# Kernel optimization log

Measured on AMD Instinct MI355X. Metric: run time of the kernel, lower is better.

## Reference

```python
import jax, jax.numpy as jnp
import numpy as np

B, T, D, K = 8, 4096, 1024, 4096

def setup_inputs() -> dict:
    key = jax.random.key(0)
    kx, kc = jax.random.split(key)
    x = jax.random.normal(kx, (B, T, D), dtype=jnp.float32)
    C = jax.random.normal(kc, (D, K), dtype=jnp.float32)  # centroids stored as [d, K]
    Cnorm = jnp.sum(C * C, axis=0, keepdims=True)  # [1, K], matches torch precompute
    return {"x": x, "C": C, "Cnorm": Cnorm}

def reference(x, C, Cnorm):
    batched = x.ndim == 3
    if batched:
        b, t, d = x.shape
        x2 = x.reshape(-1, d)  # [N, d]
    else:
        x2 = x
    dist = jnp.sum(x2 * x2, axis=1, keepdims=True) - 2.0 * (x2 @ C) + Cnorm
    assigned = jnp.argmin(dist, axis=1)
    if batched:
        assigned = assigned.reshape(b, t)
    return assigned
```

## Files before the change

### kernel.cpp

```cpp
#include <hip/hip_runtime.h>
#include <cstdint>
#include <cstddef>

typedef _Float16 half8 __attribute__((ext_vector_type(8)));
typedef _Float16 half4 __attribute__((ext_vector_type(4)));
typedef float    floatx4 __attribute__((ext_vector_type(4)));

constexpr int N_ROWS = 32768;
constexpr int D_DIM  = 1024;
constexpr int K_CENT = 4096;
constexpr int CAP    = 4096;
constexpr int KSL    = 4;
constexpr int RSL    = 8;
constexpr float EPS_GAP = 0.4f;

__device__ __forceinline__ void gload_lds16(const void* g, void* l) {
    __builtin_amdgcn_global_load_lds(
        (const __attribute__((address_space(1))) uint32_t*)g,
        (__attribute__((address_space(3))) uint32_t*)l, 16, 0, 0);
}

__global__ __launch_bounds__(256) void convert_C_kernel(
    const float* __restrict__ C, _Float16* __restrict__ ChiT, _Float16* __restrict__ CloT)
{
    __shared__ float tile[32][33];
    const int bk = blockIdx.x, bd = blockIdx.y, t = threadIdx.x;
    const int r = t >> 3, c4 = (t & 7) * 4;
    const float4 v = *(const float4*)&C[(size_t)(bd * 32 + r) * K_CENT + bk * 32 + c4];
    tile[r][c4 + 0] = v.x; tile[r][c4 + 1] = v.y;
    tile[r][c4 + 2] = v.z; tile[r][c4 + 3] = v.w;
    __syncthreads();
    half4 h, l;
#pragma unroll
    for (int i = 0; i < 4; ++i) {
        const float f = tile[c4 + i][r];
        const _Float16 hi = (_Float16)f;
        h[i] = hi;
        l[i] = (_Float16)(f - (float)hi);
    }
    *(half4*)&ChiT[(size_t)(bk * 32 + r) * D_DIM + bd * 32 + c4] = h;
    *(half4*)&CloT[(size_t)(bk * 32 + r) * D_DIM + bd * 32 + c4] = l;
}

__global__ __launch_bounds__(256) void convert_x_kernel(
    const float* __restrict__ x, _Float16* __restrict__ xh)
{
    const size_t g = (size_t)blockIdx.x * 256 + threadIdx.x;
    const float4 v0 = *(const float4*)&x[g * 8];
    const float4 v1 = *(const float4*)&x[g * 8 + 4];
    half8 h;
    h[0] = (_Float16)v0.x; h[1] = (_Float16)v0.y; h[2] = (_Float16)v0.z; h[3] = (_Float16)v0.w;
    h[4] = (_Float16)v1.x; h[5] = (_Float16)v1.y; h[6] = (_Float16)v1.z; h[7] = (_Float16)v1.w;
    *(half8*)&xh[g * 8] = h;
}

constexpr int Q_A  = 0;
constexpr int Q_B  = 4096;
constexpr int Q_HB = 8192;

__device__ __forceinline__ void stage4(
    _Float16* buf, const _Float16* __restrict__ xh, const _Float16* __restrict__ ChiT,
    int row0, int kc, int kd, int wid, int scol, int skg)
{
#pragma unroll
    for (int q = 0; q < 2; ++q) {
        const int sub = wid * 2 + q;
        gload_lds16(&xh[(size_t)(row0 + sub * 16 + scol) * D_DIM + kd + skg * 8],
                    buf + Q_A + sub * 512);
    }
#pragma unroll
    for (int q = 0; q < 2; ++q) {
        const int sub = wid * 2 + q;
        gload_lds16(&ChiT[(size_t)(kc + sub * 16 + scol) * D_DIM + kd + skg * 8],
                    buf + Q_B + sub * 512);
    }
}

__global__ __launch_bounds__(256, 3) void kmeans_pass1(
    const _Float16* __restrict__ xh, const _Float16* __restrict__ ChiT,
    const float* __restrict__ Cnorm,
    float* __restrict__ m1buf, int* __restrict__ i1buf, float* __restrict__ m2buf)
{
    __shared__ _Float16 lds[2][Q_HB];
    __shared__ float red_d[2][64][2];
    __shared__ int   red_i[2][64][2];
    __shared__ float red_2[2][64][2];

    const int bid  = blockIdx.x;
    const int xcd  = bid & 7;
    const int ks   = xcd & 3;
    const int rb   = (bid >> 3) * 2 + (xcd >> 2);
    const int row0 = rb * 128;
    const int kb0  = ks * (K_CENT / KSL);

    const int tid  = threadIdx.x;
    const int lane = tid & 63;
    const int wid  = tid >> 6;
    const int wm   = wid >> 1;
    const int wn   = wid & 1;

    const int l15 = lane & 15;
    const int l4  = lane >> 4;
    const int kge = l4 ^ ((l15 >> 1) & 3);
    const int fragoff = l15 * 32 + kge * 8;

    const int scol = lane >> 2;
    const int skg  = (lane & 3) ^ ((scol >> 1) & 3);

    float rm1 = 3.4e38f, rm2 = 3.4e38f;
    int   ri1 = 0;

    constexpr int NCH   = (K_CENT / KSL) / 128;
    constexpr int NSTEP = NCH * 32;

    stage4(lds[0], xh, ChiT, row0, kb0, 0, wid, scol, skg);

    floatx4 acc[4][4];
#pragma unroll
    for (int i = 0; i < 4; ++i)
#pragma unroll
        for (int j = 0; j < 4; ++j) acc[i][j] = (floatx4)0.0f;

    for (int s = 0; s < NSTEP; ++s) {
        _Float16* bufc = lds[s & 1];
        _Float16* bufn = lds[(s + 1) & 1];
        const int s1 = s + 1;
        if (s1 < NSTEP) {
            const int nkc = kb0 + (s1 >> 5) * 128;
            const int nkd = (s1 & 31) * 32;
            stage4(bufn, xh, ChiT, row0, nkc, nkd, wid, scol, skg);
            asm volatile("s_waitcnt vmcnt(4)" ::: "memory");
        } else {
            asm volatile("s_waitcnt vmcnt(0)" ::: "memory");
        }
        __builtin_amdgcn_s_barrier();

        half8 ah[4], bh[4];
#pragma unroll
        for (int i = 0; i < 4; ++i)
            ah[i] = *(const half8*)(bufc + Q_A + (wm * 4 + i) * 512 + fragoff);
#pragma unroll
        for (int j = 0; j < 4; ++j)
            bh[j] = *(const half8*)(bufc + Q_B + (wn * 4 + j) * 512 + fragoff);

        __builtin_amdgcn_s_setprio(1);
#pragma unroll
        for (int i = 0; i < 4; ++i)
#pragma unroll
            for (int j = 0; j < 4; ++j)
                acc[i][j] = __builtin_amdgcn_mfma_f32_16x16x32_f16(ah[i], bh[j], acc[i][j], 0, 0, 0);
        __builtin_amdgcn_s_setprio(0);

        asm volatile("" ::: "memory");
        __builtin_amdgcn_s_barrier();

        if ((s & 31) == 31) {
            const int ci   = s >> 5;
            const int colw = ci * 128 + wn * 64;
            float cn4[4];
#pragma unroll
            for (int j = 0; j < 4; ++j) cn4[j] = Cnorm[kb0 + colw + j * 16 + l15];

#pragma unroll
            for (int i = 0; i < 4; ++i)
#pragma unroll
                for (int r = 0; r < 4; ++r) {
                    float m1 = 3.4e38f, m2 = 3.4e38f;
                    int   i1 = 0;
#pragma unroll
                    for (int j = 0; j < 4; ++j) {
                        const float d  = fmaf(-2.0f, acc[i][j][r], cn4[j]);
                        const int   ix = kb0 + colw + j * 16 + l15;
                        if (d < m1) { m2 = m1; m1 = d; i1 = ix; }
                        else if (d < m2) { m2 = d; }
                    }
#pragma unroll
                    for (int off = 1; off < 16; off <<= 1) {
                        const float om1 = __shfl_xor(m1, off, 64);
                        const int   oi  = __shfl_xor(i1, off, 64);
                        const float om2 = __shfl_xor(m2, off, 64);
                        const float nm2 = fminf(fminf(m2, om2), fmaxf(m1, om1));
                        if (om1 < m1 || (om1 == m1 && oi < i1)) { m1 = om1; i1 = oi; }
                        m2 = nm2;
                    }
                    if (l15 == 0) {
                        const int rr = i * 16 + l4 * 4 + r;
                        red_d[wm][rr][wn] = m1;
                        red_i[wm][rr][wn] = i1;
                        red_2[wm][rr][wn] = m2;
                    }
                }
            asm volatile("s_waitcnt lgkmcnt(0)" ::: "memory");
            __builtin_amdgcn_s_barrier();
            __builtin_amdgcn_sched_barrier(0);

            if (tid < 128) {
                const int h2 = tid >> 6;
                const int r2 = tid & 63;
                float m1 = red_d[h2][r2][0], m2 = red_2[h2][r2][0];
                int   i1 = red_i[h2][r2][0];
                const float om1 = red_d[h2][r2][1];
                const int   oi  = red_i[h2][r2][1];
                const float om2 = red_2[h2][r2][1];
                m2 = fminf(fminf(m2, om2), fmaxf(m1, om1));
                if (om1 < m1 || (om1 == m1 && oi < i1)) { m1 = om1; i1 = oi; }
                const float nm2 = fminf(fminf(rm2, m2), fmaxf(rm1, m1));
                if (m1 < rm1 || (m1 == rm1 && i1 < ri1)) { rm1 = m1; ri1 = i1; }
                rm2 = nm2;
            }

#pragma unroll
            for (int i = 0; i < 4; ++i)
#pragma unroll
                for (int j = 0; j < 4; ++j) acc[i][j] = (floatx4)0.0f;
        }
    }

    if (tid < 128) {
        const size_t off = (size_t)ks * N_ROWS + row0 + tid;
        m1buf[off] = rm1;
        i1buf[off] = ri1;
        m2buf[off] = rm2;
    }
}

__global__ __launch_bounds__(256) void kmeans_merge4(
    const float* __restrict__ m1buf, const int* __restrict__ i1buf,
    const float* __restrict__ m2buf, int* __restrict__ out,
    int* __restrict__ urows, unsigned int* __restrict__ ucount)
{
    const int row = blockIdx.x * 256 + threadIdx.x;
    float m1 = m1buf[row], m2 = m2buf[row];
    int   i1 = i1buf[row];
#pragma unroll
    for (int s = 1; s < KSL; ++s) {
        const float om1 = m1buf[(size_t)s * N_ROWS + row];
        const float om2 = m2buf[(size_t)s * N_ROWS + row];
        const int   oi  = i1buf[(size_t)s * N_ROWS + row];
        const float nm2 = fminf(fminf(m2, om2), fmaxf(m1, om1));
        if (om1 < m1 || (om1 == m1 && oi < i1)) { m1 = om1; i1 = oi; }
        m2 = nm2;
    }
    out[row] = i1;
    if (m2 - m1 <= EPS_GAP) {
        const unsigned slot = atomicAdd(ucount, 1u);
        if (slot < (unsigned)CAP) urows[slot] = row;
    }
}

__global__ __launch_bounds__(64) void kmeans_gather(
    const float* __restrict__ x, const int* __restrict__ urows,
    const unsigned int* __restrict__ ucount,
    _Float16* __restrict__ xch, _Float16* __restrict__ xcl)
{
    const unsigned cntr = *ucount;
    const unsigned cnt = cntr > (unsigned)CAP ? (unsigned)CAP : cntr;
    const unsigned slot = blockIdx.x;
    if (slot >= cnt) return;
    const int row = urows[slot];
    const int t = threadIdx.x;
#pragma unroll
    for (int e = 0; e < 16; ++e) {
        const int idx = e * 64 + t;
        const float v = x[(size_t)row * D_DIM + idx];
        const _Float16 h = (_Float16)v;
        xch[(size_t)slot * D_DIM + idx] = h;
        xcl[(size_t)slot * D_DIM + idx] = (_Float16)(v - (float)h);
    }
}

constexpr int R_XH = 0;
constexpr int R_XL = 1024;
constexpr int R_CH = 2048;
constexpr int R_CL = 10240;
constexpr int R_HB = 18432;

__global__ __launch_bounds__(256) void kmeans_rescore2(
    const _Float16* __restrict__ xch, const _Float16* __restrict__ xcl,
    const _Float16* __restrict__ ChiT, const _Float16* __restrict__ CloT,
    const float* __restrict__ Cnorm, const unsigned int* __restrict__ ucount,
    float* __restrict__ rpd, int* __restrict__ rpi)
{
    const unsigned cntr = *ucount;
    const unsigned cnt = cntr > (unsigned)CAP ? (unsigned)CAP : cntr;
    const int bid = blockIdx.x;
    const int ksl = bid & 7;
    const int grp = bid >> 3;
    if ((unsigned)(grp * 32) >= cnt) return;

    __shared__ _Float16 lds[2][R_HB];
    __shared__ float rd[32][4];
    __shared__ int   ri[32][4];

    const int tid  = threadIdx.x;
    const int lane = tid & 63;
    const int wid  = tid >> 6;
    const int l15  = lane & 15;
    const int l4   = lane >> 4;
    const int kge  = l4 ^ ((l15 >> 1) & 3);
    const int fragoff = l15 * 32 + kge * 8;
    const int scol = lane >> 2;
    const int skg  = (lane & 3) ^ ((scol >> 1) & 3);

    const int base  = grp * 32;
    const int kbase = ksl * (K_CENT / RSL);

    float best[2][4];
    int   bidx[2][4];
#pragma unroll
    for (int i = 0; i < 2; ++i)
#pragma unroll
        for (int r = 0; r < 4; ++r) { best[i][r] = 3.4e38f; bidx[i][r] = 0; }

    for (int ch = 0; ch < 2; ++ch) {
        const int kc = kbase + ch * 256;
        floatx4 acc[2][4];
#pragma unroll
        for (int i = 0; i < 2; ++i)
#pragma unroll
            for (int j = 0; j < 4; ++j) acc[i][j] = (floatx4)0.0f;

        {
            _Float16* buf = lds[0];
#pragma unroll
            for (int q = 0; q < 4; ++q) {
                const int sub = wid * 4 + q;
                gload_lds16(&ChiT[(size_t)(kc + sub * 16 + scol) * D_DIM + 0 + skg * 8], buf + R_CH + sub * 512);
                gload_lds16(&CloT[(size_t)(kc + sub * 16 + scol) * D_DIM + 0 + skg * 8], buf + R_CL + sub * 512);
            }
            if (wid < 2)
                gload_lds16(&xch[(size_t)(base + wid * 16 + scol) * D_DIM + 0 + skg * 8], buf + R_XH + wid * 512);
            else
                gload_lds16(&xcl[(size_t)(base + (wid - 2) * 16 + scol) * D_DIM + 0 + skg * 8], buf + R_XL + (wid - 2) * 512);
            __syncthreads();
        }

        for (int kdi = 0; kdi < D_DIM / 32; ++kdi) {
            const int cur = kdi & 1;
            _Float16* bufc = lds[cur];
            _Float16* bufn = lds[cur ^ 1];
            const int  kdn = (kdi + 1) * 32;
            const bool pf  = (kdi + 1 < D_DIM / 32);

            if (pf) {
#pragma unroll
                for (int q = 0; q < 4; ++q) {
                    const int sub = wid * 4 + q;
                    gload_lds16(&ChiT[(size_t)(kc + sub * 16 + scol) * D_DIM + kdn + skg * 8], bufn + R_CH + sub * 512);
                    gload_lds16(&CloT[(size_t)(kc + sub * 16 + scol) * D_DIM + kdn + skg * 8], bufn + R_CL + sub * 512);
                }
                if (wid < 2)
                    gload_lds16(&xch[(size_t)(base + wid * 16 + scol) * D_DIM + kdn + skg * 8], bufn + R_XH + wid * 512);
                else
                    gload_lds16(&xcl[(size_t)(base + (wid - 2) * 16 + scol) * D_DIM + kdn + skg * 8], bufn + R_XL + (wid - 2) * 512);
            }

            half8 ah[2], al[2], bh[4], bl[4];
#pragma unroll
            for (int i = 0; i < 2; ++i) {
                ah[i] = *(const half8*)(bufc + R_XH + i * 512 + fragoff);
                al[i] = *(const half8*)(bufc + R_XL + i * 512 + fragoff);
            }
#pragma unroll
            for (int j = 0; j < 4; ++j) {
                bh[j] = *(const half8*)(bufc + R_CH + (wid * 4 + j) * 512 + fragoff);
                bl[j] = *(const half8*)(bufc + R_CL + (wid * 4 + j) * 512 + fragoff);
            }
#pragma unroll
            for (int i = 0; i < 2; ++i)
#pragma unroll
                for (int j = 0; j < 4; ++j) {
                    acc[i][j] = __builtin_amdgcn_mfma_f32_16x16x32_f16(ah[i], bh[j], acc[i][j], 0, 0, 0);
                    acc[i][j] = __builtin_amdgcn_mfma_f32_16x16x32_f16(ah[i], bl[j], acc[i][j], 0, 0, 0);
                    acc[i][j] = __builtin_amdgcn_mfma_f32_16x16x32_f16(al[i], bh[j], acc[i][j], 0, 0, 0);
                }
            __syncthreads();
        }

#pragma unroll
        for (int j = 0; j < 4; ++j) {
            const int col = kc + wid * 64 + j * 16 + l15;
            const float cn = Cnorm[col];
#pragma unroll
            for (int i = 0; i < 2; ++i)
#pragma unroll
                for (int r = 0; r < 4; ++r) {
                    const float d = fmaf(-2.0f, acc[i][j][r], cn);
                    if (d < best[i][r]) { best[i][r] = d; bidx[i][r] = col; }
                }
        }
    }

#pragma unroll
    for (int i = 0; i < 2; ++i)
#pragma unroll
        for (int r = 0; r < 4; ++r) {
            float m1 = best[i][r];
            int   i1 = bidx[i][r];
#pragma unroll
            for (int off = 1; off < 16; off <<= 1) {
                const float om1 = __shfl_xor(m1, off, 64);
                const int   oi  = __shfl_xor(i1, off, 64);
                if (om1 < m1 || (om1 == m1 && oi < i1)) { m1 = om1; i1 = oi; }
            }
            if (l15 == 0) { rd[i * 16 + l4 * 4 + r][wid] = m1; ri[i * 16 + l4 * 4 + r][wid] = i1; }
        }
    __syncthreads();

    if (tid < 32) {
        float m1 = rd[tid][0];
        int   i1 = ri[tid][0];
#pragma unroll
        for (int w = 1; w < 4; ++w) {
            const float om1 = rd[tid][w];
            const int   oi  = ri[tid][w];
            if (om1 < m1 || (om1 == m1 && oi < i1)) { m1 = om1; i1 = oi; }
        }
        rpd[(size_t)(base + tid) * RSL + ksl] = m1;
        rpi[(size_t)(base + tid) * RSL + ksl] = i1;
    }
}

__global__ __launch_bounds__(256) void kmeans_merge2(
    const float* __restrict__ rpd, const int* __restrict__ rpi,
    const int* __restrict__ urows, const unsigned int* __restrict__ ucount,
    int* __restrict__ out)
{
    const unsigned cntr = *ucount;
    const unsigned cnt = cntr > (unsigned)CAP ? (unsigned)CAP : cntr;
    const unsigned s = blockIdx.x * 256 + threadIdx.x;
    if (s >= cnt) return;
    float m1 = rpd[(size_t)s * RSL];
    int   i1 = rpi[(size_t)s * RSL];
#pragma unroll
    for (int k = 1; k < RSL; ++k) {
        const float om = rpd[(size_t)s * RSL + k];
        const int   oi = rpi[(size_t)s * RSL + k];
        if (om < m1 || (om == m1 && oi < i1)) { m1 = om; i1 = oi; }
    }
    out[urows[s]] = i1;
}

constexpr int F_XH = 0, F_XL = 4096, F_CH = 8192, F_CL = 16384, F_HB = 24576;

__device__ __forceinline__ void write_x2(_Float16* buf, const float4 v, int r, int kb) {
    const _Float16 h0 = (_Float16)v.x, h1 = (_Float16)v.y;
    const _Float16 h2 = (_Float16)v.z, h3 = (_Float16)v.w;
    const int kg  = kb >> 3;
    const int hs  = (kb >> 2) & 1;
    const int kge = kg ^ ((r >> 1) & 3);
    const int base = (r >> 4) * 512 + (r & 15) * 32 + kge * 8 + hs * 4;
    *(half4*)(buf + F_XH + base) = (half4){h0, h1, h2, h3};
    *(half4*)(buf + F_XL + base) = (half4){(_Float16)(v.x - (float)h0), (_Float16)(v.y - (float)h1),
                                           (_Float16)(v.z - (float)h2), (_Float16)(v.w - (float)h3)};
}

__global__ __launch_bounds__(512, 2) void kmeans_mfma_kernel(
    const float* __restrict__ x, const _Float16* __restrict__ ChiT,
    const _Float16* __restrict__ CloT, const float* __restrict__ Cnorm,
    int* __restrict__ out)
{
    __shared__ _Float16 lds[2][F_HB];
    __shared__ float red_d[2][64][4];
    __shared__ int   red_i[2][64][4];

    const int tid  = threadIdx.x;
    const int lane = tid & 63;
    const int wid  = tid >> 6;
    const int wm   = wid >> 2;
    const int wn   = wid & 3;
    const int row0 = blockIdx.x * 128;
    const int l15 = lane & 15;
    const int l4  = lane >> 4;
    const int kge = l4 ^ ((l15 >> 1) & 3);
    const int fragoff = l15 * 32 + kge * 8;
    const int sr = tid >> 2, sc = tid & 3;
    const int ccol = lane >> 2;
    const int ckg  = (lane & 3) ^ ((ccol >> 1) & 3);

    float best[4][4];
    int   bidx[4][4];
#pragma unroll
    for (int i = 0; i < 4; ++i)
#pragma unroll
        for (int r = 0; r < 4; ++r) { best[i][r] = 3.4e38f; bidx[i][r] = 0; }

    for (int kc = 0; kc < K_CENT; kc += 256) {
        floatx4 acc[4][4];
#pragma unroll
        for (int i = 0; i < 4; ++i)
#pragma unroll
            for (int j = 0; j < 4; ++j) acc[i][j] = (floatx4)0.0f;
        {
            _Float16* buf = lds[0];
            const float4 xv0 = *(const float4*)&x[(size_t)(row0 + sr) * D_DIM + 0 + sc * 4];
            const float4 xv1 = *(const float4*)&x[(size_t)(row0 + sr) * D_DIM + 16 + sc * 4];
            gload_lds16(&ChiT[(size_t)(kc + wid * 16 + ccol) * D_DIM + 0 + ckg * 8], buf + F_CH + wid * 512);
            gload_lds16(&ChiT[(size_t)(kc + (wid + 8) * 16 + ccol) * D_DIM + 0 + ckg * 8], buf + F_CH + (wid + 8) * 512);
            gload_lds16(&CloT[(size_t)(kc + wid * 16 + ccol) * D_DIM + 0 + ckg * 8], buf + F_CL + wid * 512);
            gload_lds16(&CloT[(size_t)(kc + (wid + 8) * 16 + ccol) * D_DIM + 0 + ckg * 8], buf + F_CL + (wid + 8) * 512);
            write_x2(buf, xv0, sr, sc * 4);
            write_x2(buf, xv1, sr, sc * 4 + 16);
            __syncthreads();
        }
        for (int kdi = 0; kdi < D_DIM / 32; ++kdi) {
            const int cur = kdi & 1;
            _Float16* bufc = lds[cur];
            _Float16* bufn = lds[cur ^ 1];
            const int  kdn = (kdi + 1) * 32;
            const bool pf  = (kdi + 1 < D_DIM / 32);
            float4 xv0, xv1;
            if (pf) {
                xv0 = *(const float4*)&x[(size_t)(row0 + sr) * D_DIM + kdn + sc * 4];
                xv1 = *(const float4*)&x[(size_t)(row0 + sr) * D_DIM + kdn + 16 + sc * 4];
                gload_lds16(&ChiT[(size_t)(kc + wid * 16 + ccol) * D_DIM + kdn + ckg * 8], bufn + F_CH + wid * 512);
                gload_lds16(&ChiT[(size_t)(kc + (wid + 8) * 16 + ccol) * D_DIM + kdn + ckg * 8], bufn + F_CH + (wid + 8) * 512);
                gload_lds16(&CloT[(size_t)(kc + wid * 16 + ccol) * D_DIM + kdn + ckg * 8], bufn + F_CL + wid * 512);
                gload_lds16(&CloT[(size_t)(kc + (wid + 8) * 16 + ccol) * D_DIM + kdn + ckg * 8], bufn + F_CL + (wid + 8) * 512);
            }
            half8 ah[4], al[4], bh[4], bl[4];
#pragma unroll
            for (int i = 0; i < 4; ++i) {
                ah[i] = *(const half8*)(bufc + F_XH + (wm * 4 + i) * 512 + fragoff);
                al[i] = *(const half8*)(bufc + F_XL + (wm * 4 + i) * 512 + fragoff);
            }
#pragma unroll
            for (int j = 0; j < 4; ++j) {
                bh[j] = *(const half8*)(bufc + F_CH + (wn * 4 + j) * 512 + fragoff);
                bl[j] = *(const half8*)(bufc + F_CL + (wn * 4 + j) * 512 + fragoff);
            }
#pragma unroll
            for (int i = 0; i < 4; ++i)
#pragma unroll
                for (int j = 0; j < 4; ++j) {
                    acc[i][j] = __builtin_amdgcn_mfma_f32_16x16x32_f16(ah[i], bh[j], acc[i][j], 0, 0, 0);
                    acc[i][j] = __builtin_amdgcn_mfma_f32_16x16x32_f16(ah[i], bl[j], acc[i][j], 0, 0, 0);
                    acc[i][j] = __builtin_amdgcn_mfma_f32_16x16x32_f16(al[i], bh[j], acc[i][j], 0, 0, 0);
                }
            if (pf) {
                write_x2(bufn, xv0, sr, sc * 4);
                write_x2(bufn, xv1, sr, sc * 4 + 16);
            }
            __syncthreads();
        }
        const int colw = kc + wn * 64;
#pragma unroll
        for (int ns = 0; ns < 4; ++ns) {
            const float cn = Cnorm[colw + ns * 16 + l15];
            const int   ix = colw + ns * 16 + l15;
#pragma unroll
            for (int i = 0; i < 4; ++i)
#pragma unroll
                for (int r = 0; r < 4; ++r) {
                    const float d = fmaf(-2.0f, acc[i][ns][r], cn);
                    if (d < best[i][r]) { best[i][r] = d; bidx[i][r] = ix; }
                }
        }
    }
#pragma unroll
    for (int i = 0; i < 4; ++i)
#pragma unroll
        for (int r = 0; r < 4; ++r) {
            float d  = best[i][r];
            int   ix = bidx[i][r];
#pragma unroll
            for (int off = 1; off < 16; off <<= 1) {
                const float od = __shfl_xor(d, off, 64);
                const int   oi = __shfl_xor(ix, off, 64);
                if (od < d || (od == d && oi < ix)) { d = od; ix = oi; }
            }
            if (l15 == 0) {
                red_d[wm][i * 16 + l4 * 4 + r][wn] = d;
                red_i[wm][i * 16 + l4 * 4 + r][wn] = ix;
            }
        }
    __syncthreads();
    if (tid < 128) {
        const int hh = tid >> 6, rr = tid & 63;
        float bd = red_d[hh][rr][0];
        int   bi2 = red_i[hh][rr][0];
#pragma unroll
        for (int w = 1; w < 4; ++w) {
            const float od = red_d[hh][rr][w];
            const int   oi = red_i[hh][rr][w];
            if (od < bd || (od == bd && oi < bi2)) { bd = od; bi2 = oi; }
        }
        out[row0 + tid] = bi2;
    }
}

__global__ __launch_bounds__(256, 2) void kmeans_assign_f32(
    const float* __restrict__ x, const float* __restrict__ Cm,
    const float* __restrict__ Cnorm, int* __restrict__ out)
{
    __shared__ float xs[32][64];
    __shared__ float cs[32][64];
    const int tid = threadIdx.x;
    const int tx = tid & 15, ty = tid >> 4;
    const int row0 = blockIdx.x * 64;
    const int xr = tid >> 3, xc = tid & 7;
    const int cr = tid >> 4, cc = tid & 15;
    float best[4]; int bidx[4];
#pragma unroll
    for (int i = 0; i < 4; ++i) { best[i] = 3.4e38f; bidx[i] = 0; }
    for (int kc = 0; kc < K_CENT; kc += 64) {
        float acc[16];
#pragma unroll
        for (int i = 0; i < 16; ++i) acc[i] = 0.0f;
        for (int kd = 0; kd < D_DIM; kd += 32) {
            const float4 xv0 = *(const float4*)&x[(size_t)(row0 + xr) * D_DIM + kd + xc * 4];
            const float4 xv1 = *(const float4*)&x[(size_t)(row0 + xr + 32) * D_DIM + kd + xc * 4];
            const float4 cv0 = *(const float4*)&Cm[(size_t)(kd + cr) * K_CENT + kc + cc * 4];
            const float4 cv1 = *(const float4*)&Cm[(size_t)(kd + cr + 16) * K_CENT + kc + cc * 4];
            __syncthreads();
            xs[xc*4+0][xr] = xv0.x; xs[xc*4+1][xr] = xv0.y; xs[xc*4+2][xr] = xv0.z; xs[xc*4+3][xr] = xv0.w;
            xs[xc*4+0][xr+32] = xv1.x; xs[xc*4+1][xr+32] = xv1.y; xs[xc*4+2][xr+32] = xv1.z; xs[xc*4+3][xr+32] = xv1.w;
            *(float4*)&cs[cr][cc*4]    = cv0;
            *(float4*)&cs[cr+16][cc*4] = cv1;
            __syncthreads();
#pragma unroll
            for (int kk = 0; kk < 32; ++kk) {
                const float4 a = *(const float4*)&xs[kk][ty*4];
                const float4 b = *(const float4*)&cs[kk][tx*4];
                acc[ 0] += a.x*b.x; acc[ 1] += a.x*b.y; acc[ 2] += a.x*b.z; acc[ 3] += a.x*b.w;
                acc[ 4] += a.y*b.x; acc[ 5] += a.y*b.y; acc[ 6] += a.y*b.z; acc[ 7] += a.y*b.w;
                acc[ 8] += a.z*b.x; acc[ 9] += a.z*b.y; acc[10] += a.z*b.z; acc[11] += a.z*b.w;
                acc[12] += a.w*b.x; acc[13] += a.w*b.y; acc[14] += a.w*b.z; acc[15] += a.w*b.w;
            }
        }
        const float4 cn = *(const float4*)&Cnorm[kc + tx*4];
        const float cnv[4] = {cn.x, cn.y, cn.z, cn.w};
#pragma unroll
        for (int i = 0; i < 4; ++i)
#pragma unroll
            for (int j = 0; j < 4; ++j) {
                const float dist = cnv[j] - 2.0f * acc[i*4+j];
                const int   idx  = kc + tx*4 + j;
                if (dist < best[i]) { best[i] = dist; bidx[i] = idx; }
            }
    }
#pragma unroll
    for (int i = 0; i < 4; ++i) {
        float d = best[i]; int ix = bidx[i];
#pragma unroll
        for (int off = 1; off < 16; off <<= 1) {
            const float od = __shfl_xor(d, off, 64);
            const int   oi = __shfl_xor(ix, off, 64);
            if (od < d || (od == d && oi < ix)) { d = od; ix = oi; }
        }
        if (tx == 0) out[row0 + ty*4 + i] = ix;
    }
}

extern "C" void kernel_launch(void* const* d_in, const int* in_sizes, int n_in,
                              void* d_out, int out_size, void* d_ws, size_t ws_size,
                              hipStream_t stream) {
    const float* x     = (const float*)d_in[0];
    const float* C     = (const float*)d_in[1];
    const float* Cnorm = (const float*)d_in[2];
    int* out = (int*)d_out;

    const size_t chalf = (size_t)K_CENT * D_DIM;
    const size_t capd  = (size_t)CAP * D_DIM;
    const size_t xhN   = (size_t)N_ROWS * D_DIM;

    const size_t sz_base = (2 * chalf + 2 * capd) * 2
                         + (size_t)KSL * N_ROWS * 12
                         + (size_t)CAP * RSL * 8
                         + (size_t)CAP * 4 + 64;
    const size_t need_full = sz_base + xhN * 2;
    const size_t need_r3   = 2 * chalf * 2;

    if (ws_size >= need_full) {
        _Float16* ChiT = (_Float16*)d_ws;
        _Float16* CloT = ChiT + chalf;
        _Float16* xch  = CloT + chalf;
        _Float16* xcl  = xch + capd;
        float* m1buf = (float*)(xcl + capd);
        float* m2buf = m1buf + (size_t)KSL * N_ROWS;
        int*   i1buf = (int*)(m2buf + (size_t)KSL * N_ROWS);
        float* rpd   = (float*)(i1buf + (size_t)KSL * N_ROWS);
        int*   rpi   = (int*)(rpd + (size_t)CAP * RSL);
        int*   urows = rpi + (size_t)CAP * RSL;
        unsigned int* ucount = (unsigned int*)(urows + CAP);
        _Float16* xh = (_Float16*)(ucount + 16);

        convert_C_kernel<<<dim3(128, 32), 256, 0, stream>>>(C, ChiT, CloT);
        convert_x_kernel<<<dim3((int)(xhN / 2048)), 256, 0, stream>>>(x, xh);
        hipMemsetAsync(ucount, 0, sizeof(unsigned int), stream);
        kmeans_pass1<<<dim3(256 * KSL), 256, 0, stream>>>(xh, ChiT, Cnorm, m1buf, i1buf, m2buf);
        kmeans_merge4<<<dim3(N_ROWS / 256), 256, 0, stream>>>(m1buf, i1buf, m2buf, out, urows, ucount);
        kmeans_gather<<<dim3(CAP), 64, 0, stream>>>(x, urows, ucount, xch, xcl);
        kmeans_rescore2<<<dim3((CAP / 32) * RSL), 256, 0, stream>>>(xch, xcl, ChiT, CloT, Cnorm, ucount, rpd, rpi);
        kmeans_merge2<<<dim3(CAP / 256), 256, 0, stream>>>(rpd, rpi, urows, ucount, out);
    } else if (ws_size >= need_r3) {
        _Float16* ChiT = (_Float16*)d_ws;
        _Float16* CloT = ChiT + chalf;
        convert_C_kernel<<<dim3(128, 32), 256, 0, stream>>>(C, ChiT, CloT);
        kmeans_mfma_kernel<<<dim3(N_ROWS / 128), 512, 0, stream>>>(x, ChiT, CloT, Cnorm, out);
    } else {
        kmeans_assign_f32<<<dim3(N_ROWS / 64), 256, 0, stream>>>(x, C, Cnorm, out);
    }
}
```

Baseline: 501.8 us.

## Load MFMA fragments directly from global memory, drop LDS double buffering

Replaces the LDS-staged, double-buffered global_load_lds pipeline in pass1 with direct per-wave global loads of the A and B fragments, relying on L1/L2 for reuse. It also raises the occupancy hint from 3 to 4 blocks per SIMD. This removes LDS traffic and the two barriers per k-step. In exchange, each wave now issues redundant global loads for data that was previously shared across the four waves, so latency hiding depends on occupancy and the caches.

```diff
diff --git a/kernel.cpp b/kernel.cpp
--- a/kernel.cpp
+++ b/kernel.cpp
@@ -54,34 +54,11 @@
     *(half8*)&xh[g * 8] = h;
 }
 
-constexpr int Q_A  = 0;
-constexpr int Q_B  = 4096;
-constexpr int Q_HB = 8192;
-
-__device__ __forceinline__ void stage4(
-    _Float16* buf, const _Float16* __restrict__ xh, const _Float16* __restrict__ ChiT,
-    int row0, int kc, int kd, int wid, int scol, int skg)
-{
-#pragma unroll
-    for (int q = 0; q < 2; ++q) {
-        const int sub = wid * 2 + q;
-        gload_lds16(&xh[(size_t)(row0 + sub * 16 + scol) * D_DIM + kd + skg * 8],
-                    buf + Q_A + sub * 512);
-    }
-#pragma unroll
-    for (int q = 0; q < 2; ++q) {
-        const int sub = wid * 2 + q;
-        gload_lds16(&ChiT[(size_t)(kc + sub * 16 + scol) * D_DIM + kd + skg * 8],
-                    buf + Q_B + sub * 512);
-    }
-}
-
-__global__ __launch_bounds__(256, 3) void kmeans_pass1(
+__global__ __launch_bounds__(256, 4) void kmeans_pass1(
     const _Float16* __restrict__ xh, const _Float16* __restrict__ ChiT,
     const float* __restrict__ Cnorm,
     float* __restrict__ m1buf, int* __restrict__ i1buf, float* __restrict__ m2buf)
 {
-    __shared__ _Float16 lds[2][Q_HB];
     __shared__ float red_d[2][64][2];
     __shared__ int   red_i[2][64][2];
     __shared__ float red_2[2][64][2];
@@ -101,119 +78,95 @@
 
     const int l15 = lane & 15;
     const int l4  = lane >> 4;
-    const int kge = l4 ^ ((l15 >> 1) & 3);
-    const int fragoff = l15 * 32 + kge * 8;
-
-    const int scol = lane >> 2;
-    const int skg  = (lane & 3) ^ ((scol >> 1) & 3);
+
+    const _Float16* paB = xh   + (size_t)(row0 + wm * 64 + l15) * D_DIM + l4 * 8;
+    const _Float16* pbB = ChiT + (size_t)(kb0  + wn * 64 + l15) * D_DIM + l4 * 8;
 
     float rm1 = 3.4e38f, rm2 = 3.4e38f;
     int   ri1 = 0;
 
-    constexpr int NCH   = (K_CENT / KSL) / 128;
-    constexpr int NSTEP = NCH * 32;
-
-    stage4(lds[0], xh, ChiT, row0, kb0, 0, wid, scol, skg);
-
-    floatx4 acc[4][4];
-#pragma unroll
-    for (int i = 0; i < 4; ++i)
-#pragma unroll
-        for (int j = 0; j < 4; ++j) acc[i][j] = (floatx4)0.0f;
-
-    for (int s = 0; s < NSTEP; ++s) {
-        _Float16* bufc = lds[s & 1];
-        _Float16* bufn = lds[(s + 1) & 1];
-        const int s1 = s + 1;
-        if (s1 < NSTEP) {
-            const int nkc = kb0 + (s1 >> 5) * 128;
-            const int nkd = (s1 & 31) * 32;
-            stage4(bufn, xh, ChiT, row0, nkc, nkd, wid, scol, skg);
-            asm volatile("s_waitcnt vmcnt(4)" ::: "memory");
-        } else {
-            asm volatile("s_waitcnt vmcnt(0)" ::: "memory");
-        }
-        __builtin_amdgcn_s_barrier();
-
-        half8 ah[4], bh[4];
+    constexpr int NCH = (K_CENT / KSL) / 128;
+
+    for (int ci = 0; ci < NCH; ++ci) {
+        const _Float16* pb = pbB + (size_t)ci * 128 * D_DIM;
+
+        floatx4 acc[4][4];
 #pragma unroll
         for (int i = 0; i < 4; ++i)
-            ah[i] = *(const half8*)(bufc + Q_A + (wm * 4 + i) * 512 + fragoff);
-#pragma unroll
-        for (int j = 0; j < 4; ++j)
-            bh[j] = *(const half8*)(bufc + Q_B + (wn * 4 + j) * 512 + fragoff);
-
-        __builtin_amdgcn_s_setprio(1);
+#pragma unroll
+            for (int j = 0; j < 4; ++j) acc[i][j] = (floatx4)0.0f;
+
+#pragma unroll 4
+        for (int kdi = 0; kdi < 32; ++kdi) {
+            const int kd = kdi * 32;
+            half8 ah[4], bh[4];
+#pragma unroll
+            for (int i = 0; i < 4; ++i)
+                ah[i] = *(const half8*)(paB + (size_t)i * 16 * D_DIM + kd);
+#pragma unroll
+            for (int j = 0; j < 4; ++j)
+                bh[j] = *(const half8*)(pb + (size_t)j * 16 * D_DIM + kd);
+
+            __builtin_amdgcn_s_setprio(1);
+#pragma unroll
+            for (int i = 0; i < 4; ++i)
+#pragma unroll
+                for (int j = 0; j < 4; ++j)
+                    acc[i][j] = __builtin_amdgcn_mfma_f32_16x16x32_f16(ah[i], bh[j], acc[i][j], 0, 0, 0);
+            __builtin_amdgcn_s_setprio(0);
+        }
+
+        const int colw = ci * 128 + wn * 64;
+        float cn4[4];
+#pragma unroll
+        for (int j = 0; j < 4; ++j) cn4[j] = Cnorm[kb0 + colw + j * 16 + l15];
+
 #pragma unroll
         for (int i = 0; i < 4; ++i)
 #pragma unroll
-            for (int j = 0; j < 4; ++j)
-                acc[i][j] = __builtin_amdgcn_mfma_f32_16x16x32_f16(ah[i], bh[j], acc[i][j], 0, 0, 0);
-        __builtin_amdgcn_s_setprio(0);
-
-        asm volatile("" ::: "memory");
-        __builtin_amdgcn_s_barrier();
-
-        if ((s & 31) == 31) {
-            const int ci   = s >> 5;
-            const int colw = ci * 128 + wn * 64;
-            float cn4[4];
-#pragma unroll
-            for (int j = 0; j < 4; ++j) cn4[j] = Cnorm[kb0 + colw + j * 16 + l15];
-
-#pragma unroll
-            for (int i = 0; i < 4; ++i)
-#pragma unroll
-                for (int r = 0; r < 4; ++r) {
-                    float m1 = 3.4e38f, m2 = 3.4e38f;
-                    int   i1 = 0;
-#pragma unroll
-                    for (int j = 0; j < 4; ++j) {
-                        const float d  = fmaf(-2.0f, acc[i][j][r], cn4[j]);
-                        const int   ix = kb0 + colw + j * 16 + l15;
-                        if (d < m1) { m2 = m1; m1 = d; i1 = ix; }
-                        else if (d < m2) { m2 = d; }
-                    }
-#pragma unroll
-                    for (int off = 1; off < 16; off <<= 1) {
-                        const float om1 = __shfl_xor(m1, off, 64);
-                        const int   oi  = __shfl_xor(i1, off, 64);
-                        const float om2 = __shfl_xor(m2, off, 64);
-                        const float nm2 = fminf(fminf(m2, om2), fmaxf(m1, om1));
-                        if (om1 < m1 || (om1 == m1 && oi < i1)) { m1 = om1; i1 = oi; }
-                        m2 = nm2;
-                    }
-                    if (l15 == 0) {
-                        const int rr = i * 16 + l4 * 4 + r;
-                        red_d[wm][rr][wn] = m1;
-                        red_i[wm][rr][wn] = i1;
-                        red_2[wm][rr][wn] = m2;
-                    }
-                }
-            asm volatile("s_waitcnt lgkmcnt(0)" ::: "memory");
-            __builtin_amdgcn_s_barrier();
-            __builtin_amdgcn_sched_barrier(0);
-
-            if (tid < 128) {
-                const int h2 = tid >> 6;
-                const int r2 = tid & 63;
-                float m1 = red_d[h2][r2][0], m2 = red_2[h2][r2][0];
-                int   i1 = red_i[h2][r2][0];
-                const float om1 = red_d[h2][r2][1];
-                const int   oi  = red_i[h2][r2][1];
-                const float om2 = red_2[h2][r2][1];
-                m2 = fminf(fminf(m2, om2), fmaxf(m1, om1));
-                if (om1 < m1 || (om1 == m1 && oi < i1)) { m1 = om1; i1 = oi; }
-                const float nm2 = fminf(fminf(rm2, m2), fmaxf(rm1, m1));
-                if (m1 < rm1 || (m1 == rm1 && i1 < ri1)) { rm1 = m1; ri1 = i1; }
-                rm2 = nm2;
-            }
-
-#pragma unroll
-            for (int i = 0; i < 4; ++i)
-#pragma unroll
-                for (int j = 0; j < 4; ++j) acc[i][j] = (floatx4)0.0f;
-        }
+            for (int r = 0; r < 4; ++r) {
+                float m1 = 3.4e38f, m2 = 3.4e38f;
+                int   i1 = 0;
+#pragma unroll
+                for (int j = 0; j < 4; ++j) {
+                    const float d  = fmaf(-2.0f, acc[i][j][r], cn4[j]);
+                    const int   ix = kb0 + colw + j * 16 + l15;
+                    if (d < m1) { m2 = m1; m1 = d; i1 = ix; }
+                    else if (d < m2) { m2 = d; }
+                }
+#pragma unroll
+                for (int off = 1; off < 16; off <<= 1) {
+                    const float om1 = __shfl_xor(m1, off, 64);
+                    const int   oi  = __shfl_xor(i1, off, 64);
+                    const float om2 = __shfl_xor(m2, off, 64);
+                    const float nm2 = fminf(fminf(m2, om2), fmaxf(m1, om1));
+                    if (om1 < m1 || (om1 == m1 && oi < i1)) { m1 = om1; i1 = oi; }
+                    m2 = nm2;
+                }
+                if (l15 == 0) {
+                    const int rr = i * 16 + l4 * 4 + r;
+                    red_d[wm][rr][wn] = m1;
+                    red_i[wm][rr][wn] = i1;
+                    red_2[wm][rr][wn] = m2;
+                }
+            }
+        __syncthreads();
+
+        if (tid < 128) {
+            const int h2 = tid >> 6;
+            const int r2 = tid & 63;
+            float m1 = red_d[h2][r2][0], m2 = red_2[h2][r2][0];
+            int   i1 = red_i[h2][r2][0];
+            const float om1 = red_d[h2][r2][1];
+            const int   oi  = red_i[h2][r2][1];
+            const float om2 = red_2[h2][r2][1];
+            m2 = fminf(fminf(m2, om2), fmaxf(m1, om1));
+            if (om1 < m1 || (om1 == m1 && oi < i1)) { m1 = om1; i1 = oi; }
+            const float nm2 = fminf(fminf(rm2, m2), fmaxf(rm1, m1));
+            if (m1 < rm1 || (m1 == rm1 && i1 < ri1)) { rm1 = m1; ri1 = i1; }
+            rm2 = nm2;
+        }
+        __syncthreads();
     }
 
     if (tid < 128) {
```

New measurement: 1.079 ms. 2.15x slower.
